# Performance work log

Hardware: AMD Instinct MI355X
Metric: run time of the kernel (lower is better)

Reference implementation:

```python
import jax, jax.numpy as jnp
import numpy as np

EMBED = 1024
B, I, J = 8, 2048, 2048
SCALE = EMBED ** -0.5


def setup_inputs() -> dict:
    key = jax.random.key(0)
    ks = jax.random.split(key, 5)
    s = EMBED ** -0.5  # init scale for weights
    return {
        "q_in": jax.random.normal(ks[0], (B, I, EMBED), dtype=jnp.float32),
        "k_v": jax.random.normal(ks[1], (B, J, EMBED), dtype=jnp.float32),
        "Wq": jax.random.normal(ks[2], (EMBED, EMBED), dtype=jnp.float32) * s,
        "bq": jnp.zeros((EMBED,), dtype=jnp.float32),
        "Wk": jax.random.normal(ks[3], (EMBED, EMBED), dtype=jnp.float32) * s,
        "bk": jnp.zeros((EMBED,), dtype=jnp.float32),
        "Wv": jax.random.normal(ks[4], (EMBED, EMBED), dtype=jnp.float32) * s,
        "bv": jnp.zeros((EMBED,), dtype=jnp.float32),
    }


def reference(q_in, k_v, Wq, bq, Wk, bk, Wv, bv):
    # Linear projections (torch Linear: x @ W.T + b; here W stored as [in, out])
    q = q_in @ Wq + bq            # [b, i, d]
    k = k_v @ Wk + bk             # [b, j, d]
    v = k_v @ Wv + bv             # [b, j, d]
    sim = jnp.einsum('bid,bjd->bij', q, k) * SCALE  # [b, i, j]
    attn = jax.nn.softmax(sim, axis=-1)
    # dropout with drop_rate=0.0 is identity
    out = jnp.einsum('bij,bjd->bid', attn, v)       # [b, i, d]
    return out
```

## Files before the change

### kernel.cpp

```cpp
#include <hip/hip_runtime.h>
#include <hip/hip_bf16.h>


#define BATCH 8
#define SEQ   2048
#define EMB   1024
#define SC2   0.045084222f

typedef __attribute__((ext_vector_type(8))) short bf16x8;
typedef __attribute__((ext_vector_type(4))) float f32x4;
typedef __attribute__((ext_vector_type(4))) unsigned short u16x4;
typedef __attribute__((ext_vector_type(8))) unsigned short u16x8;
typedef __attribute__((ext_vector_type(4))) float fl4;

__device__ __forceinline__ unsigned short f2bf(float f) {
    unsigned u = __builtin_bit_cast(unsigned, f);
    unsigned r = u + 0x7fffu + ((u >> 16) & 1u);
    return (unsigned short)(r >> 16);
}
__device__ __forceinline__ float bf2f(unsigned short s) {
    return __builtin_bit_cast(float, ((unsigned)s) << 16);
}
__device__ __forceinline__ void gload16(const unsigned short* g, unsigned short* l) {
    __builtin_amdgcn_global_load_lds(
        (const __attribute__((address_space(1))) void*)g,
        (__attribute__((address_space(3))) void*)l, 16, 0, 0);
}

__global__ __launch_bounds__(256)
void convert_all(const float* __restrict__ q_in, const float* __restrict__ k_v,
                 const float* __restrict__ Wq, const float* __restrict__ Wk,
                 const float* __restrict__ Wv,
                 unsigned short* __restrict__ qbin, unsigned short* __restrict__ kvbin,
                 unsigned short* __restrict__ Wt)
{
    const int bid = blockIdx.x;
    const int tid = threadIdx.x;
    if (bid < 4096) {
        const size_t N = (size_t)BATCH * SEQ * EMB;
        size_t idx = ((size_t)bid * 256 + tid) * 8;
        const size_t stride = (size_t)4096 * 256 * 8;
        for (; idx < N; idx += stride) {
            fl4 a0 = *(const fl4*)&q_in[idx];
            fl4 a1 = *(const fl4*)&q_in[idx + 4];
            fl4 b0 = *(const fl4*)&k_v[idx];
            fl4 b1 = *(const fl4*)&k_v[idx + 4];
            u16x8 ua, ub;
#pragma unroll
            for (int i = 0; i < 4; i++) {
                ua[i] = f2bf(a0[i]); ua[i + 4] = f2bf(a1[i]);
                ub[i] = f2bf(b0[i]); ub[i + 4] = f2bf(b1[i]);
            }
            *(u16x8*)&qbin[idx] = ua;
            *(u16x8*)&kvbin[idx] = ub;
        }
    } else {
        const int b2 = bid - 4096;
        const int wsel = b2 >> 8, rest = b2 & 255;
        const float* W = (wsel == 0) ? Wq : (wsel == 1) ? Wk : Wv;
        unsigned short* O = Wt + (size_t)wsel * EMB * EMB;
        const int k0 = (rest >> 4) * 64;
        const int n0 = (rest & 15) * 64;
        __shared__ unsigned short l[64 * 65];
#pragma unroll
        for (int it = 0; it < 16; it++) {
            const int lin = it * 256 + tid;
            const int k = lin >> 6, n = lin & 63;
            l[n * 65 + k] = f2bf(W[(size_t)(k0 + k) * EMB + n0 + n]);
        }
        __syncthreads();
#pragma unroll
        for (int it = 0; it < 16; it++) {
            const int lin = it * 256 + tid;
            const int n = lin >> 6, k = lin & 63;
            O[(size_t)(n0 + n) * EMB + k0 + k] = l[n * 65 + k];
        }
    }
}

__device__ __forceinline__ void stageT(const unsigned short* lanebase, size_t rstride,
                                       unsigned short* lwave) {
#pragma unroll
    for (int i = 0; i < 2; i++)
        gload16(lanebase + (size_t)(i * 128) * rstride, lwave + i * 4096);
}

#define PIPE_TILE(SLOT, DO_STAGE, STAGE_A_BASE, STAGE_A_LDS, STAGE_B_BASE, STAGE_B_LDS) \
    {                                                                           \
        const unsigned short* pa = &sA[SLOT][0];                                \
        const unsigned short* pb = &sB[SLOT][0];                                \
        bf16x8 a0 = *(bf16x8*)&pa[aoff0];                                       \
        bf16x8 a1 = *(bf16x8*)&pa[aoff0 + 512];                                 \
        bf16x8 a2 = *(bf16x8*)&pa[aoff0 + 1024];                                \
        bf16x8 a3 = *(bf16x8*)&pa[aoff0 + 1536];                                \
        bf16x8 a4 = *(bf16x8*)&pa[aoff0 + 2048];                                \
        bf16x8 a5 = *(bf16x8*)&pa[aoff0 + 2560];                                \
        bf16x8 a6 = *(bf16x8*)&pa[aoff0 + 3072];                                \
        bf16x8 a7 = *(bf16x8*)&pa[aoff0 + 3584];                                \
        bf16x8 bv0 = *(bf16x8*)&pb[boff0];                                      \
        bf16x8 bv1 = *(bf16x8*)&pb[boff0 + 512];                                \
        bf16x8 bv2 = *(bf16x8*)&pb[boff0 + 1024];                               \
        bf16x8 bv3 = *(bf16x8*)&pb[boff0 + 1536];                               \
        if (DO_STAGE) stageT(STAGE_A_BASE, strideA, STAGE_A_LDS);               \
        __builtin_amdgcn_s_setprio(1);                                          \
        acc[0][0] = __builtin_amdgcn_mfma_f32_16x16x32_bf16(a0, bv0, acc[0][0], 0, 0, 0); \
        acc[0][1] = __builtin_amdgcn_mfma_f32_16x16x32_bf16(a0, bv1, acc[0][1], 0, 0, 0); \
        acc[0][2] = __builtin_amdgcn_mfma_f32_16x16x32_bf16(a0, bv2, acc[0][2], 0, 0, 0); \
        acc[0][3] = __builtin_amdgcn_mfma_f32_16x16x32_bf16(a0, bv3, acc[0][3], 0, 0, 0); \
        acc[1][0] = __builtin_amdgcn_mfma_f32_16x16x32_bf16(a1, bv0, acc[1][0], 0, 0, 0); \
        acc[1][1] = __builtin_amdgcn_mfma_f32_16x16x32_bf16(a1, bv1, acc[1][1], 0, 0, 0); \
        acc[1][2] = __builtin_amdgcn_mfma_f32_16x16x32_bf16(a1, bv2, acc[1][2], 0, 0, 0); \
        acc[1][3] = __builtin_amdgcn_mfma_f32_16x16x32_bf16(a1, bv3, acc[1][3], 0, 0, 0); \
        acc[2][0] = __builtin_amdgcn_mfma_f32_16x16x32_bf16(a2, bv0, acc[2][0], 0, 0, 0); \
        acc[2][1] = __builtin_amdgcn_mfma_f32_16x16x32_bf16(a2, bv1, acc[2][1], 0, 0, 0); \
        acc[2][2] = __builtin_amdgcn_mfma_f32_16x16x32_bf16(a2, bv2, acc[2][2], 0, 0, 0); \
        acc[2][3] = __builtin_amdgcn_mfma_f32_16x16x32_bf16(a2, bv3, acc[2][3], 0, 0, 0); \
        acc[3][0] = __builtin_amdgcn_mfma_f32_16x16x32_bf16(a3, bv0, acc[3][0], 0, 0, 0); \
        acc[3][1] = __builtin_amdgcn_mfma_f32_16x16x32_bf16(a3, bv1, acc[3][1], 0, 0, 0); \
        acc[3][2] = __builtin_amdgcn_mfma_f32_16x16x32_bf16(a3, bv2, acc[3][2], 0, 0, 0); \
        acc[3][3] = __builtin_amdgcn_mfma_f32_16x16x32_bf16(a3, bv3, acc[3][3], 0, 0, 0); \
        __builtin_amdgcn_s_setprio(0);                                          \
        if (DO_STAGE) stageT(STAGE_B_BASE, strideB, STAGE_B_LDS);               \
        __builtin_amdgcn_s_setprio(1);                                          \
        acc[4][0] = __builtin_amdgcn_mfma_f32_16x16x32_bf16(a4, bv0, acc[4][0], 0, 0, 0); \
        acc[4][1] = __builtin_amdgcn_mfma_f32_16x16x32_bf16(a4, bv1, acc[4][1], 0, 0, 0); \
        acc[4][2] = __builtin_amdgcn_mfma_f32_16x16x32_bf16(a4, bv2, acc[4][2], 0, 0, 0); \
        acc[4][3] = __builtin_amdgcn_mfma_f32_16x16x32_bf16(a4, bv3, acc[4][3], 0, 0, 0); \
        acc[5][0] = __builtin_amdgcn_mfma_f32_16x16x32_bf16(a5, bv0, acc[5][0], 0, 0, 0); \
        acc[5][1] = __builtin_amdgcn_mfma_f32_16x16x32_bf16(a5, bv1, acc[5][1], 0, 0, 0); \
        acc[5][2] = __builtin_amdgcn_mfma_f32_16x16x32_bf16(a5, bv2, acc[5][2], 0, 0, 0); \
        acc[5][3] = __builtin_amdgcn_mfma_f32_16x16x32_bf16(a5, bv3, acc[5][3], 0, 0, 0); \
        acc[6][0] = __builtin_amdgcn_mfma_f32_16x16x32_bf16(a6, bv0, acc[6][0], 0, 0, 0); \
        acc[6][1] = __builtin_amdgcn_mfma_f32_16x16x32_bf16(a6, bv1, acc[6][1], 0, 0, 0); \
        acc[6][2] = __builtin_amdgcn_mfma_f32_16x16x32_bf16(a6, bv2, acc[6][2], 0, 0, 0); \
        acc[6][3] = __builtin_amdgcn_mfma_f32_16x16x32_bf16(a6, bv3, acc[6][3], 0, 0, 0); \
        acc[7][0] = __builtin_amdgcn_mfma_f32_16x16x32_bf16(a7, bv0, acc[7][0], 0, 0, 0); \
        acc[7][1] = __builtin_amdgcn_mfma_f32_16x16x32_bf16(a7, bv1, acc[7][1], 0, 0, 0); \
        acc[7][2] = __builtin_amdgcn_mfma_f32_16x16x32_bf16(a7, bv2, acc[7][2], 0, 0, 0); \
        acc[7][3] = __builtin_amdgcn_mfma_f32_16x16x32_bf16(a7, bv3, acc[7][3], 0, 0, 0); \
        __builtin_amdgcn_s_setprio(0);                                          \
        asm volatile("s_waitcnt vmcnt(4)" ::: "memory");                        \
        __builtin_amdgcn_s_barrier();                                           \
        __builtin_amdgcn_sched_barrier(0);                                      \
    }

__device__ __forceinline__ void pipe_gemm(
    const unsigned short* __restrict__ Asrc,
    const unsigned short* __restrict__ Bsrc,
    const size_t strideA, const size_t strideB, const int NT,
    unsigned short (*sA)[8192], unsigned short (*sB)[8192],
    const int lwave, const int aoff0, const int boff0,
    f32x4 acc[8][4])
{
    stageT(Asrc, strideA, &sA[0][lwave]);
    stageT(Bsrc, strideB, &sB[0][lwave]);
    stageT(Asrc + 32, strideA, &sA[1][lwave]);
    stageT(Bsrc + 32, strideB, &sB[1][lwave]);
    asm volatile("s_waitcnt vmcnt(4)" ::: "memory");
    __builtin_amdgcn_s_barrier();
    __builtin_amdgcn_sched_barrier(0);

    for (int T = 0; T < NT; ++T) {
        const int s = T & 3;
        const int doStage = (T + 2 < NT);
        const int s2 = (T + 2) & 3;
        PIPE_TILE(s, doStage, Asrc + (T + 2) * 32, &sA[s2][lwave],
                  Bsrc + (T + 2) * 32, &sB[s2][lwave]);
    }
}

#define PIPE_PREAMBLE                                                     \
    __shared__ unsigned short sMem[65536];                    \
    unsigned short (*sA)[8192] = (unsigned short (*)[8192])sMem;          \
    unsigned short (*sB)[8192] = (unsigned short (*)[8192])(sMem + 32768);\
    const int tid = threadIdx.x, lane = tid & 63;                         \
    const int wid = tid >> 6, wr = wid >> 2, wn = wid & 3;                \
    const int r = lane & 15, g = lane >> 4;                               \
    const int lwave = (wid << 9);                                         \
    const int scol = ((tid & 3) ^ ((tid >> 3) & 3)) * 8;                  \
    const int gsw = (g ^ ((r >> 1) & 3)) * 8;                             \
    const int aoff0 = (wr * 128 + r) * 32 + gsw;                          \
    const int boff0 = (wn * 64 + r) * 32 + gsw;                           \
    f32x4 acc[8][4];                                                      \
    _Pragma("unroll") for (int i_ = 0; i_ < 8; i_++)                      \
    _Pragma("unroll") for (int j_ = 0; j_ < 4; j_++) acc[i_][j_] = (f32x4)0.0f;

__device__ __forceinline__ void lds_flush_bf16(const unsigned short* sP,
                                               unsigned short* gbase,
                                               size_t gstride, int tid)
{
    const int lane = tid & 63, wv = tid >> 6;
    const int rowsel = lane >> 5, jj = lane & 31;
#pragma unroll
    for (int it = 0; it < 16; ++it) {
        const int row = it * 16 + wv * 2 + rowsel;
        const int byte = row * 512 + ((jj * 16) ^ ((row & 7) << 4));
        u16x8 v = *(const u16x8*)((const char*)sP + byte);
        *(u16x8*)&gbase[(size_t)row * gstride + jj * 8] = v;
    }
}

__global__ __launch_bounds__(512, 1)
void proj_all(const unsigned short* __restrict__ Wt,
              const unsigned short* __restrict__ qbin,
              const unsigned short* __restrict__ kvbin,
              const float* __restrict__ bq, const float* __restrict__ bk,
              const float* __restrict__ bv,
              unsigned short* __restrict__ qb, unsigned short* __restrict__ kb,
              unsigned short* __restrict__ vt)
{
    PIPE_PREAMBLE
    const int bid = blockIdx.x;
    const size_t strideA = EMB, strideB = EMB;
    const unsigned short* Asrc;
    const unsigned short* Bsrc;
    int d0 = 0, i0 = 0, m0 = 0, n0 = 0;
    const bool qrole = (bid < 256);
    if (qrole) {
        const int lid = (bid & 7) * 32 + (bid >> 3);
        d0 = (lid & 3) * 256; i0 = (lid >> 2) * 256;
        Asrc = Wt + (size_t)(d0 + (tid >> 2)) * EMB + scol;
        Bsrc = qbin + (size_t)(i0 + (tid >> 2)) * EMB + scol;
    } else {
        const int b2 = bid - 256;
        const int lid = (b2 & 7) * 64 + (b2 >> 3);
        n0 = (lid & 7) * 256; m0 = (lid >> 3) * 256;
        Asrc = kvbin + (size_t)(m0 + (tid >> 2)) * EMB + scol;
        Bsrc = Wt + (size_t)EMB * EMB + (size_t)(n0 + (tid >> 2)) * EMB + scol;
    }

    pipe_gemm(Asrc, Bsrc, strideA, strideB, EMB / 32, sA, sB, lwave, aoff0, boff0, acc);

    if (qrole) {
#pragma unroll
        for (int mm = 0; mm < 8; mm++) {
            const int colb = wr * 128 + mm * 16 + g * 4;
            const fl4 b4 = *(const fl4*)&bq[d0 + colb];
#pragma unroll
            for (int n = 0; n < 4; n++) {
                const int row = wn * 64 + n * 16 + r;
                u16x4 u;
#pragma unroll
                for (int c = 0; c < 4; c++) u[c] = f2bf(acc[mm][n][c] + b4[c]);
                const int byte = row * 512 + ((colb * 2) ^ ((row & 7) << 4));
                *(u16x4*)((char*)sMem + byte) = u;
            }
        }
        __syncthreads();
        lds_flush_bf16(sMem, qb + (size_t)i0 * EMB + d0, EMB, tid);
    } else {
        const int b = m0 >> 11;
        const int j0l = m0 & 2047;
        if (n0 < 1024) {
#pragma unroll
            for (int mm = 0; mm < 8; mm++) {
                const int ibase = m0 + wr * 128 + mm * 16 + g * 4;
#pragma unroll
                for (int n = 0; n < 4; n++) {
                    const int col = n0 + wn * 64 + n * 16 + r;
                    const float bb = bk[col];
#pragma unroll
                    for (int c = 0; c < 4; c++)
                        kb[(size_t)(ibase + c) * EMB + col] = f2bf(acc[mm][n][c] + bb);
                }
            }
        } else {
#pragma unroll
            for (int mm = 0; mm < 8; mm++) {
                const int colb = wr * 128 + mm * 16 + g * 4;
#pragma unroll
                for (int n = 0; n < 4; n++) {
                    const int row = wn * 64 + n * 16 + r;
                    const float bb = bv[n0 - 1024 + row];
                    u16x4 u;
#pragma unroll
                    for (int c = 0; c < 4; c++) u[c] = f2bf(acc[mm][n][c] + bb);
                    const int byte = row * 512 + ((colb * 2) ^ ((row & 7) << 4));
                    *(u16x4*)((char*)sMem + byte) = u;
                }
            }
            __syncthreads();
            lds_flush_bf16(sMem, vt + ((size_t)b * EMB + (n0 - 1024)) * SEQ + j0l,
                           SEQ, tid);
        }
    }
}

__global__ __launch_bounds__(512, 1)
void qk256_kernel(const unsigned short* __restrict__ qb,
                  const unsigned short* __restrict__ kb,
                  unsigned short* __restrict__ P,
                  float* __restrict__ Ppart)
{
    PIPE_PREAMBLE
    const int bid = blockIdx.x;
    const int lid = (bid & 7) * 64 + (bid >> 3);
    const int b = lid >> 6, jt = (lid >> 3) & 7, it = lid & 7;
    const int j0 = jt * 256, i0 = it * 256;
    const size_t strideA = EMB, strideB = EMB;
    const unsigned short* Ag = kb + (size_t)b * SEQ * EMB;
    const unsigned short* Bg = qb + (size_t)b * SEQ * EMB;
    const unsigned short* Asrc = Ag + (size_t)(j0 + (tid >> 2)) * EMB + scol;
    const unsigned short* Bsrc = Bg + (size_t)(i0 + (tid >> 2)) * EMB + scol;

    pipe_gemm(Asrc, Bsrc, strideA, strideB, EMB / 32, sA, sB, lwave, aoff0, boff0, acc);

    float ps[4] = {0.f, 0.f, 0.f, 0.f};
#pragma unroll
    for (int mm = 0; mm < 8; mm++) {
        const int colb = wr * 128 + mm * 16 + g * 4;
#pragma unroll
        for (int n = 0; n < 4; n++) {
            const int row = wn * 64 + n * 16 + r;
            u16x4 u;
#pragma unroll
            for (int c = 0; c < 4; c++) {
                const float p = exp2f(acc[mm][n][c] * SC2);
                ps[n] += p;
                u[c] = f2bf(p);
            }
            const int byte = row * 512 + ((colb * 2) ^ ((row & 7) << 4));
            *(u16x4*)((char*)sMem + byte) = u;
        }
    }
#pragma unroll
    for (int n = 0; n < 4; n++) {
        ps[n] += __shfl_xor(ps[n], 16);
        ps[n] += __shfl_xor(ps[n], 32);
    }
    if (g == 0) {
        const int slot = jt * 2 + wr;
        float* pp = Ppart + (size_t)slot * (BATCH * SEQ) + (size_t)b * SEQ;
#pragma unroll
        for (int n = 0; n < 4; n++)
            pp[i0 + wn * 64 + n * 16 + r] = ps[n];
    }
    __syncthreads();
    unsigned short* Pb = P + (size_t)b * SEQ * SEQ;
    lds_flush_bf16(sMem, Pb + (size_t)i0 * SEQ + j0, SEQ, tid);
}

__global__ __launch_bounds__(512, 1)
void pv256_kernel(const unsigned short* __restrict__ P,
                  const unsigned short* __restrict__ vt,
                  const float* __restrict__ Ppart,
                  float* __restrict__ out)
{
    PIPE_PREAMBLE
    const int bid = blockIdx.x;
    const int lid = (bid & 7) * 32 + (bid >> 3);
    const int b = lid >> 5, it = (lid >> 2) & 7, dt = lid & 3;
    const int d0 = dt * 256, i0 = it * 256;
    const size_t strideA = SEQ, strideB = SEQ;
    const unsigned short* Ag = vt + (size_t)b * EMB * SEQ;
    const unsigned short* Bg = P + (size_t)b * SEQ * SEQ;
    const unsigned short* Asrc = Ag + (size_t)(d0 + (tid >> 2)) * SEQ + scol;
    const unsigned short* Bsrc = Bg + (size_t)(i0 + (tid >> 2)) * SEQ + scol;

    float inv[4];
#pragma unroll
    for (int n = 0; n < 4; n++) {
        const int row = b * SEQ + i0 + wn * 64 + n * 16 + r;
        float s = 0.f;
#pragma unroll
        for (int slot = 0; slot < 16; slot++)
            s += Ppart[(size_t)slot * (BATCH * SEQ) + row];
        inv[n] = 1.0f / s;
    }

    pipe_gemm(Asrc, Bsrc, strideA, strideB, SEQ / 32, sA, sB, lwave, aoff0, boff0, acc);

    float* ob = out + (size_t)b * SEQ * EMB;
    float* sF = (float*)sMem;
#pragma unroll
    for (int h = 0; h < 2; h++) {
        if (wr == h) {
#pragma unroll
            for (int mm = 0; mm < 8; mm++) {
                const int colb = mm * 16 + g * 4;
#pragma unroll
                for (int n = 0; n < 4; n++) {
                    const int row = wn * 64 + n * 16 + r;
                    fl4 o;
#pragma unroll
                    for (int c = 0; c < 4; c++) o[c] = acc[mm][n][c] * inv[n];
                    const int byte = row * 512 + ((colb * 4) ^ ((row & 7) << 4));
                    *(fl4*)((char*)sF + byte) = o;
                }
            }
        }
        __syncthreads();
        {
            const int rowsel = lane >> 5, jj = lane & 31;
#pragma unroll
            for (int itx = 0; itx < 16; ++itx) {
                const int row = itx * 16 + wid * 2 + rowsel;
                const int byte = row * 512 + ((jj * 16) ^ ((row & 7) << 4));
                fl4 v = *(const fl4*)((const char*)sF + byte);
                *(fl4*)&ob[(size_t)(i0 + row) * EMB + d0 + h * 128 + jj * 4] = v;
            }
        }
        if (h == 0) __syncthreads();
    }
}

extern "C" void kernel_launch(void* const* d_in, const int* in_sizes, int n_in,
                              void* d_out, int out_size, void* d_ws, size_t ws_size,
                              hipStream_t stream)
{
    const float* q_in = (const float*)d_in[0];
    const float* k_v  = (const float*)d_in[1];
    const float* Wq   = (const float*)d_in[2];
    const float* bq   = (const float*)d_in[3];
    const float* Wk   = (const float*)d_in[4];
    const float* bk   = (const float*)d_in[5];
    const float* Wv   = (const float*)d_in[6];
    const float* bv   = (const float*)d_in[7];
    float* out = (float*)d_out;

    char* ws = (char*)d_ws;
    unsigned short* qbin = (unsigned short*)(ws);
    unsigned short* kvbin= (unsigned short*)(ws + (size_t)33554432);
    unsigned short* P    = (unsigned short*)(ws);
    unsigned short* qb   = (unsigned short*)(ws + (size_t)67108864);
    unsigned short* kb   = (unsigned short*)(ws + (size_t)100663296);
    unsigned short* vt   = (unsigned short*)(ws + (size_t)134217728);
    unsigned short* Wt   = (unsigned short*)(ws + (size_t)167772160);
    float*          Ppart= (float*)(ws + (size_t)174063616);

    convert_all<<<4864, 256, 0, stream>>>(q_in, k_v, Wq, Wk, Wv, qbin, kvbin, Wt);
    proj_all<<<768, 512, 0, stream>>>(Wt, qbin, kvbin, bq, bk, bv, qb, kb, vt);
    qk256_kernel<<<512, 512, 0, stream>>>(qb, kb, P, Ppart);
    pv256_kernel<<<256, 512, 0, stream>>>(P, vt, Ppart, out);
}
```

Before: 293.9 us.

## Deepen GEMM pipeline with register-prefetched LDS fragments and three-tile global prefetch

Restructures the pipelined GEMM loop. The next tile's A and B fragments are read from LDS into registers during the current tile's MFMAs, ping-ponging between two register sets with the loop unrolled by two. Global-to-LDS staging now runs three tiles ahead instead of two, with both A and B issued together before the MFMA block. The aim is to hide LDS read latency and global load latency behind matrix math, at the cost of about 64 extra VGPRs and an assumption that the tile count is even.

```diff
diff --git a/kernel.cpp b/kernel.cpp
--- a/kernel.cpp
+++ b/kernel.cpp
@@ -85,59 +85,64 @@
         gload16(lanebase + (size_t)(i * 128) * rstride, lwave + i * 4096);
 }
 
-#define PIPE_TILE(SLOT, DO_STAGE, STAGE_A_BASE, STAGE_A_LDS, STAGE_B_BASE, STAGE_B_LDS) \
+#define PIPE_TILE(T, CA0,CA1,CA2,CA3,CB0,CB1,CB2,CB3,                           \
+                     NA0,NA1,NA2,NA3,NB0,NB1,NB2,NB3)                           \
     {                                                                           \
-        const unsigned short* pa = &sA[SLOT][0];                                \
-        const unsigned short* pb = &sB[SLOT][0];                                \
-        bf16x8 a0 = *(bf16x8*)&pa[aoff0];                                       \
-        bf16x8 a1 = *(bf16x8*)&pa[aoff0 + 512];                                 \
-        bf16x8 a2 = *(bf16x8*)&pa[aoff0 + 1024];                                \
-        bf16x8 a3 = *(bf16x8*)&pa[aoff0 + 1536];                                \
-        bf16x8 a4 = *(bf16x8*)&pa[aoff0 + 2048];                                \
-        bf16x8 a5 = *(bf16x8*)&pa[aoff0 + 2560];                                \
-        bf16x8 a6 = *(bf16x8*)&pa[aoff0 + 3072];                                \
-        bf16x8 a7 = *(bf16x8*)&pa[aoff0 + 3584];                                \
-        bf16x8 bv0 = *(bf16x8*)&pb[boff0];                                      \
-        bf16x8 bv1 = *(bf16x8*)&pb[boff0 + 512];                                \
-        bf16x8 bv2 = *(bf16x8*)&pb[boff0 + 1024];                               \
-        bf16x8 bv3 = *(bf16x8*)&pb[boff0 + 1536];                               \
-        if (DO_STAGE) stageT(STAGE_A_BASE, strideA, STAGE_A_LDS);               \
+        const int sc_ = (T) & 3, sn_ = ((T) + 1) & 3, ss_ = ((T) + 3) & 3;      \
+        const unsigned short* pc_ = &sA[sc_][0];                                \
+        bf16x8 x4 = *(bf16x8*)&pc_[aoff0 + 2048];                               \
+        bf16x8 x5 = *(bf16x8*)&pc_[aoff0 + 2560];                               \
+        bf16x8 x6 = *(bf16x8*)&pc_[aoff0 + 3072];                               \
+        bf16x8 x7 = *(bf16x8*)&pc_[aoff0 + 3584];                               \
+        if ((T) + 1 < NT) {                                                     \
+            const unsigned short* pa_ = &sA[sn_][0];                            \
+            const unsigned short* pb_ = &sB[sn_][0];                            \
+            NA0 = *(bf16x8*)&pa_[aoff0];                                        \
+            NA1 = *(bf16x8*)&pa_[aoff0 + 512];                                  \
+            NA2 = *(bf16x8*)&pa_[aoff0 + 1024];                                 \
+            NA3 = *(bf16x8*)&pa_[aoff0 + 1536];                                 \
+            NB0 = *(bf16x8*)&pb_[boff0];                                        \
+            NB1 = *(bf16x8*)&pb_[boff0 + 512];                                  \
+            NB2 = *(bf16x8*)&pb_[boff0 + 1024];                                 \
+            NB3 = *(bf16x8*)&pb_[boff0 + 1536];                                 \
+        }                                                                       \
+        if ((T) + 3 < NT) {                                                     \
+            stageT(Asrc + ((T) + 3) * 32, strideA, &sA[ss_][lwave]);            \
+            stageT(Bsrc + ((T) + 3) * 32, strideB, &sB[ss_][lwave]);            \
+        }                                                                       \
         __builtin_amdgcn_s_setprio(1);                                          \
-        acc[0][0] = __builtin_amdgcn_mfma_f32_16x16x32_bf16(a0, bv0, acc[0][0], 0, 0, 0); \
-        acc[0][1] = __builtin_amdgcn_mfma_f32_16x16x32_bf16(a0, bv1, acc[0][1], 0, 0, 0); \
-        acc[0][2] = __builtin_amdgcn_mfma_f32_16x16x32_bf16(a0, bv2, acc[0][2], 0, 0, 0); \
-        acc[0][3] = __builtin_amdgcn_mfma_f32_16x16x32_bf16(a0, bv3, acc[0][3], 0, 0, 0); \
-        acc[1][0] = __builtin_amdgcn_mfma_f32_16x16x32_bf16(a1, bv0, acc[1][0], 0, 0, 0); \
-        acc[1][1] = __builtin_amdgcn_mfma_f32_16x16x32_bf16(a1, bv1, acc[1][1], 0, 0, 0); \
-        acc[1][2] = __builtin_amdgcn_mfma_f32_16x16x32_bf16(a1, bv2, acc[1][2], 0, 0, 0); \
-        acc[1][3] = __builtin_amdgcn_mfma_f32_16x16x32_bf16(a1, bv3, acc[1][3], 0, 0, 0); \
-        acc[2][0] = __builtin_amdgcn_mfma_f32_16x16x32_bf16(a2, bv0, acc[2][0], 0, 0, 0); \
-        acc[2][1] = __builtin_amdgcn_mfma_f32_16x16x32_bf16(a2, bv1, acc[2][1], 0, 0, 0); \
-        acc[2][2] = __builtin_amdgcn_mfma_f32_16x16x32_bf16(a2, bv2, acc[2][2], 0, 0, 0); \
-        acc[2][3] = __builtin_amdgcn_mfma_f32_16x16x32_bf16(a2, bv3, acc[2][3], 0, 0, 0); \
-        acc[3][0] = __builtin_amdgcn_mfma_f32_16x16x32_bf16(a3, bv0, acc[3][0], 0, 0, 0); \
-        acc[3][1] = __builtin_amdgcn_mfma_f32_16x16x32_bf16(a3, bv1, acc[3][1], 0, 0, 0); \
-        acc[3][2] = __builtin_amdgcn_mfma_f32_16x16x32_bf16(a3, bv2, acc[3][2], 0, 0, 0); \
-        acc[3][3] = __builtin_amdgcn_mfma_f32_16x16x32_bf16(a3, bv3, acc[3][3], 0, 0, 0); \
-        __builtin_amdgcn_s_setprio(0);                                          \
-        if (DO_STAGE) stageT(STAGE_B_BASE, strideB, STAGE_B_LDS);               \
-        __builtin_amdgcn_s_setprio(1);                                          \
-        acc[4][0] = __builtin_amdgcn_mfma_f32_16x16x32_bf16(a4, bv0, acc[4][0], 0, 0, 0); \
-        acc[4][1] = __builtin_amdgcn_mfma_f32_16x16x32_bf16(a4, bv1, acc[4][1], 0, 0, 0); \
-        acc[4][2] = __builtin_amdgcn_mfma_f32_16x16x32_bf16(a4, bv2, acc[4][2], 0, 0, 0); \
-        acc[4][3] = __builtin_amdgcn_mfma_f32_16x16x32_bf16(a4, bv3, acc[4][3], 0, 0, 0); \
-        acc[5][0] = __builtin_amdgcn_mfma_f32_16x16x32_bf16(a5, bv0, acc[5][0], 0, 0, 0); \
-        acc[5][1] = __builtin_amdgcn_mfma_f32_16x16x32_bf16(a5, bv1, acc[5][1], 0, 0, 0); \
-        acc[5][2] = __builtin_amdgcn_mfma_f32_16x16x32_bf16(a5, bv2, acc[5][2], 0, 0, 0); \
-        acc[5][3] = __builtin_amdgcn_mfma_f32_16x16x32_bf16(a5, bv3, acc[5][3], 0, 0, 0); \
-        acc[6][0] = __builtin_amdgcn_mfma_f32_16x16x32_bf16(a6, bv0, acc[6][0], 0, 0, 0); \
-        acc[6][1] = __builtin_amdgcn_mfma_f32_16x16x32_bf16(a6, bv1, acc[6][1], 0, 0, 0); \
-        acc[6][2] = __builtin_amdgcn_mfma_f32_16x16x32_bf16(a6, bv2, acc[6][2], 0, 0, 0); \
-        acc[6][3] = __builtin_amdgcn_mfma_f32_16x16x32_bf16(a6, bv3, acc[6][3], 0, 0, 0); \
-        acc[7][0] = __builtin_amdgcn_mfma_f32_16x16x32_bf16(a7, bv0, acc[7][0], 0, 0, 0); \
-        acc[7][1] = __builtin_amdgcn_mfma_f32_16x16x32_bf16(a7, bv1, acc[7][1], 0, 0, 0); \
-        acc[7][2] = __builtin_amdgcn_mfma_f32_16x16x32_bf16(a7, bv2, acc[7][2], 0, 0, 0); \
-        acc[7][3] = __builtin_amdgcn_mfma_f32_16x16x32_bf16(a7, bv3, acc[7][3], 0, 0, 0); \
+        acc[0][0] = __builtin_amdgcn_mfma_f32_16x16x32_bf16(CA0, CB0, acc[0][0], 0, 0, 0); \
+        acc[0][1] = __builtin_amdgcn_mfma_f32_16x16x32_bf16(CA0, CB1, acc[0][1], 0, 0, 0); \
+        acc[0][2] = __builtin_amdgcn_mfma_f32_16x16x32_bf16(CA0, CB2, acc[0][2], 0, 0, 0); \
+        acc[0][3] = __builtin_amdgcn_mfma_f32_16x16x32_bf16(CA0, CB3, acc[0][3], 0, 0, 0); \
+        acc[1][0] = __builtin_amdgcn_mfma_f32_16x16x32_bf16(CA1, CB0, acc[1][0], 0, 0, 0); \
+        acc[1][1] = __builtin_amdgcn_mfma_f32_16x16x32_bf16(CA1, CB1, acc[1][1], 0, 0, 0); \
+        acc[1][2] = __builtin_amdgcn_mfma_f32_16x16x32_bf16(CA1, CB2, acc[1][2], 0, 0, 0); \
+        acc[1][3] = __builtin_amdgcn_mfma_f32_16x16x32_bf16(CA1, CB3, acc[1][3], 0, 0, 0); \
+        acc[2][0] = __builtin_amdgcn_mfma_f32_16x16x32_bf16(CA2, CB0, acc[2][0], 0, 0, 0); \
+        acc[2][1] = __builtin_amdgcn_mfma_f32_16x16x32_bf16(CA2, CB1, acc[2][1], 0, 0, 0); \
+        acc[2][2] = __builtin_amdgcn_mfma_f32_16x16x32_bf16(CA2, CB2, acc[2][2], 0, 0, 0); \
+        acc[2][3] = __builtin_amdgcn_mfma_f32_16x16x32_bf16(CA2, CB3, acc[2][3], 0, 0, 0); \
+        acc[3][0] = __builtin_amdgcn_mfma_f32_16x16x32_bf16(CA3, CB0, acc[3][0], 0, 0, 0); \
+        acc[3][1] = __builtin_amdgcn_mfma_f32_16x16x32_bf16(CA3, CB1, acc[3][1], 0, 0, 0); \
+        acc[3][2] = __builtin_amdgcn_mfma_f32_16x16x32_bf16(CA3, CB2, acc[3][2], 0, 0, 0); \
+        acc[3][3] = __builtin_amdgcn_mfma_f32_16x16x32_bf16(CA3, CB3, acc[3][3], 0, 0, 0); \
+        acc[4][0] = __builtin_amdgcn_mfma_f32_16x16x32_bf16(x4, CB0, acc[4][0], 0, 0, 0); \
+        acc[4][1] = __builtin_amdgcn_mfma_f32_16x16x32_bf16(x4, CB1, acc[4][1], 0, 0, 0); \
+        acc[4][2] = __builtin_amdgcn_mfma_f32_16x16x32_bf16(x4, CB2, acc[4][2], 0, 0, 0); \
+        acc[4][3] = __builtin_amdgcn_mfma_f32_16x16x32_bf16(x4, CB3, acc[4][3], 0, 0, 0); \
+        acc[5][0] = __builtin_amdgcn_mfma_f32_16x16x32_bf16(x5, CB0, acc[5][0], 0, 0, 0); \
+        acc[5][1] = __builtin_amdgcn_mfma_f32_16x16x32_bf16(x5, CB1, acc[5][1], 0, 0, 0); \
+        acc[5][2] = __builtin_amdgcn_mfma_f32_16x16x32_bf16(x5, CB2, acc[5][2], 0, 0, 0); \
+        acc[5][3] = __builtin_amdgcn_mfma_f32_16x16x32_bf16(x5, CB3, acc[5][3], 0, 0, 0); \
+        acc[6][0] = __builtin_amdgcn_mfma_f32_16x16x32_bf16(x6, CB0, acc[6][0], 0, 0, 0); \
+        acc[6][1] = __builtin_amdgcn_mfma_f32_16x16x32_bf16(x6, CB1, acc[6][1], 0, 0, 0); \
+        acc[6][2] = __builtin_amdgcn_mfma_f32_16x16x32_bf16(x6, CB2, acc[6][2], 0, 0, 0); \
+        acc[6][3] = __builtin_amdgcn_mfma_f32_16x16x32_bf16(x6, CB3, acc[6][3], 0, 0, 0); \
+        acc[7][0] = __builtin_amdgcn_mfma_f32_16x16x32_bf16(x7, CB0, acc[7][0], 0, 0, 0); \
+        acc[7][1] = __builtin_amdgcn_mfma_f32_16x16x32_bf16(x7, CB1, acc[7][1], 0, 0, 0); \
+        acc[7][2] = __builtin_amdgcn_mfma_f32_16x16x32_bf16(x7, CB2, acc[7][2], 0, 0, 0); \
+        acc[7][3] = __builtin_amdgcn_mfma_f32_16x16x32_bf16(x7, CB3, acc[7][3], 0, 0, 0); \
         __builtin_amdgcn_s_setprio(0);                                          \
         asm volatile("s_waitcnt vmcnt(4)" ::: "memory");                        \
         __builtin_amdgcn_s_barrier();                                           \
@@ -152,20 +157,31 @@
     const int lwave, const int aoff0, const int boff0,
     f32x4 acc[8][4])
 {
-    stageT(Asrc, strideA, &sA[0][lwave]);
-    stageT(Bsrc, strideB, &sB[0][lwave]);
+    stageT(Asrc,      strideA, &sA[0][lwave]);
+    stageT(Bsrc,      strideB, &sB[0][lwave]);
     stageT(Asrc + 32, strideA, &sA[1][lwave]);
     stageT(Bsrc + 32, strideB, &sB[1][lwave]);
+    stageT(Asrc + 64, strideA, &sA[2][lwave]);
+    stageT(Bsrc + 64, strideB, &sB[2][lwave]);
     asm volatile("s_waitcnt vmcnt(4)" ::: "memory");
     __builtin_amdgcn_s_barrier();
     __builtin_amdgcn_sched_barrier(0);
 
-    for (int T = 0; T < NT; ++T) {
-        const int s = T & 3;
-        const int doStage = (T + 2 < NT);
-        const int s2 = (T + 2) & 3;
-        PIPE_TILE(s, doStage, Asrc + (T + 2) * 32, &sA[s2][lwave],
-                  Bsrc + (T + 2) * 32, &sB[s2][lwave]);
+    bf16x8 Pa0, Pa1, Pa2, Pa3, Pb0, Pb1, Pb2, Pb3;
+    bf16x8 Qa0, Qa1, Qa2, Qa3, Qb0, Qb1, Qb2, Qb3;
+    {
+        const unsigned short* pa = &sA[0][0];
+        const unsigned short* pb = &sB[0][0];
+        Pa0 = *(bf16x8*)&pa[aoff0];        Pa1 = *(bf16x8*)&pa[aoff0 + 512];
+        Pa2 = *(bf16x8*)&pa[aoff0 + 1024]; Pa3 = *(bf16x8*)&pa[aoff0 + 1536];
+        Pb0 = *(bf16x8*)&pb[boff0];        Pb1 = *(bf16x8*)&pb[boff0 + 512];
+        Pb2 = *(bf16x8*)&pb[boff0 + 1024]; Pb3 = *(bf16x8*)&pb[boff0 + 1536];
+    }
+    for (int T = 0; T < NT; T += 2) {
+        PIPE_TILE(T,     Pa0,Pa1,Pa2,Pa3,Pb0,Pb1,Pb2,Pb3,
+                         Qa0,Qa1,Qa2,Qa3,Qb0,Qb1,Qb2,Qb3);
+        PIPE_TILE(T + 1, Qa0,Qa1,Qa2,Qa3,Qb0,Qb1,Qb2,Qb3,
+                         Pa0,Pa1,Pa2,Pa3,Pb0,Pb1,Pb2,Pb3);
     }
 }
 
```

Result: slower. 308.9 us (+5.1%).

## Fuse fp32-to-bf16 activation conversion into projection GEMM loader

Applied to the files above, without the earlier changes.

Drops the separate pass that converted q_in and k_v to bf16. The projection GEMM now loads fp32 activations into registers, packs them with v_cvt_pk_bf16_f32, and writes them to LDS inside a new mixed pipeline. Weights are still staged through the async global-to-LDS path. This removes a full read and write of the activation tensors, at the cost of a more complex register-staged pipeline with twice the global read bytes per tile. The last pipeline tile now waits for vmcnt(0), so the drain is also fixed.

```diff
diff --git a/kernel.cpp b/kernel.cpp
--- a/kernel.cpp
+++ b/kernel.cpp
@@ -11,6 +11,7 @@
 typedef __attribute__((ext_vector_type(4))) float f32x4;
 typedef __attribute__((ext_vector_type(4))) unsigned short u16x4;
 typedef __attribute__((ext_vector_type(8))) unsigned short u16x8;
+typedef __attribute__((ext_vector_type(4))) unsigned int u32x4;
 typedef __attribute__((ext_vector_type(4))) float fl4;
 
 __device__ __forceinline__ unsigned short f2bf(float f) {
@@ -21,6 +22,11 @@
 __device__ __forceinline__ float bf2f(unsigned short s) {
     return __builtin_bit_cast(float, ((unsigned)s) << 16);
 }
+__device__ __forceinline__ unsigned cvtpk(float a, float b) {
+    unsigned r;
+    asm("v_cvt_pk_bf16_f32 %0, %1, %2" : "=v"(r) : "v"(a), "v"(b));
+    return r;
+}
 __device__ __forceinline__ void gload16(const unsigned short* g, unsigned short* l) {
     __builtin_amdgcn_global_load_lds(
         (const __attribute__((address_space(1))) void*)g,
@@ -28,53 +34,28 @@
 }
 
 __global__ __launch_bounds__(256)
-void convert_all(const float* __restrict__ q_in, const float* __restrict__ k_v,
-                 const float* __restrict__ Wq, const float* __restrict__ Wk,
-                 const float* __restrict__ Wv,
-                 unsigned short* __restrict__ qbin, unsigned short* __restrict__ kvbin,
-                 unsigned short* __restrict__ Wt)
-{
-    const int bid = blockIdx.x;
+void convert_w(const float* __restrict__ Wq, const float* __restrict__ Wk,
+               const float* __restrict__ Wv, unsigned short* __restrict__ Wt)
+{
+    const int wsel = blockIdx.y;
+    const float* W = (wsel == 0) ? Wq : (wsel == 1) ? Wk : Wv;
+    unsigned short* O = Wt + (size_t)wsel * EMB * EMB;
+    const int k0 = (blockIdx.x >> 4) * 64;
+    const int n0 = (blockIdx.x & 15) * 64;
+    __shared__ unsigned short l[64 * 65];
     const int tid = threadIdx.x;
-    if (bid < 4096) {
-        const size_t N = (size_t)BATCH * SEQ * EMB;
-        size_t idx = ((size_t)bid * 256 + tid) * 8;
-        const size_t stride = (size_t)4096 * 256 * 8;
-        for (; idx < N; idx += stride) {
-            fl4 a0 = *(const fl4*)&q_in[idx];
-            fl4 a1 = *(const fl4*)&q_in[idx + 4];
-            fl4 b0 = *(const fl4*)&k_v[idx];
-            fl4 b1 = *(const fl4*)&k_v[idx + 4];
-            u16x8 ua, ub;
-#pragma unroll
-            for (int i = 0; i < 4; i++) {
-                ua[i] = f2bf(a0[i]); ua[i + 4] = f2bf(a1[i]);
-                ub[i] = f2bf(b0[i]); ub[i + 4] = f2bf(b1[i]);
-            }
-            *(u16x8*)&qbin[idx] = ua;
-            *(u16x8*)&kvbin[idx] = ub;
-        }
-    } else {
-        const int b2 = bid - 4096;
-        const int wsel = b2 >> 8, rest = b2 & 255;
-        const float* W = (wsel == 0) ? Wq : (wsel == 1) ? Wk : Wv;
-        unsigned short* O = Wt + (size_t)wsel * EMB * EMB;
-        const int k0 = (rest >> 4) * 64;
-        const int n0 = (rest & 15) * 64;
-        __shared__ unsigned short l[64 * 65];
-#pragma unroll
-        for (int it = 0; it < 16; it++) {
-            const int lin = it * 256 + tid;
-            const int k = lin >> 6, n = lin & 63;
-            l[n * 65 + k] = f2bf(W[(size_t)(k0 + k) * EMB + n0 + n]);
-        }
-        __syncthreads();
-#pragma unroll
-        for (int it = 0; it < 16; it++) {
-            const int lin = it * 256 + tid;
-            const int n = lin >> 6, k = lin & 63;
-            O[(size_t)(n0 + n) * EMB + k0 + k] = l[n * 65 + k];
-        }
+#pragma unroll
+    for (int it = 0; it < 16; it++) {
+        const int lin = it * 256 + tid;
+        const int k = lin >> 6, n = lin & 63;
+        l[n * 65 + k] = f2bf(W[(size_t)(k0 + k) * EMB + n0 + n]);
+    }
+    __syncthreads();
+#pragma unroll
+    for (int it = 0; it < 16; it++) {
+        const int lin = it * 256 + tid;
+        const int n = lin >> 6, k = lin & 63;
+        O[(size_t)(n0 + n) * EMB + k0 + k] = l[n * 65 + k];
     }
 }
 
@@ -85,8 +66,43 @@
         gload16(lanebase + (size_t)(i * 128) * rstride, lwave + i * 4096);
 }
 
-#define PIPE_TILE(SLOT, DO_STAGE, STAGE_A_BASE, STAGE_A_LDS, STAGE_B_BASE, STAGE_B_LDS) \
-    {                                                                           \
+#define MFMA16_LO(A0,A1,A2,A3)                                                  \
+        acc[0][0] = __builtin_amdgcn_mfma_f32_16x16x32_bf16(A0, bv0, acc[0][0], 0, 0, 0); \
+        acc[0][1] = __builtin_amdgcn_mfma_f32_16x16x32_bf16(A0, bv1, acc[0][1], 0, 0, 0); \
+        acc[0][2] = __builtin_amdgcn_mfma_f32_16x16x32_bf16(A0, bv2, acc[0][2], 0, 0, 0); \
+        acc[0][3] = __builtin_amdgcn_mfma_f32_16x16x32_bf16(A0, bv3, acc[0][3], 0, 0, 0); \
+        acc[1][0] = __builtin_amdgcn_mfma_f32_16x16x32_bf16(A1, bv0, acc[1][0], 0, 0, 0); \
+        acc[1][1] = __builtin_amdgcn_mfma_f32_16x16x32_bf16(A1, bv1, acc[1][1], 0, 0, 0); \
+        acc[1][2] = __builtin_amdgcn_mfma_f32_16x16x32_bf16(A1, bv2, acc[1][2], 0, 0, 0); \
+        acc[1][3] = __builtin_amdgcn_mfma_f32_16x16x32_bf16(A1, bv3, acc[1][3], 0, 0, 0); \
+        acc[2][0] = __builtin_amdgcn_mfma_f32_16x16x32_bf16(A2, bv0, acc[2][0], 0, 0, 0); \
+        acc[2][1] = __builtin_amdgcn_mfma_f32_16x16x32_bf16(A2, bv1, acc[2][1], 0, 0, 0); \
+        acc[2][2] = __builtin_amdgcn_mfma_f32_16x16x32_bf16(A2, bv2, acc[2][2], 0, 0, 0); \
+        acc[2][3] = __builtin_amdgcn_mfma_f32_16x16x32_bf16(A2, bv3, acc[2][3], 0, 0, 0); \
+        acc[3][0] = __builtin_amdgcn_mfma_f32_16x16x32_bf16(A3, bv0, acc[3][0], 0, 0, 0); \
+        acc[3][1] = __builtin_amdgcn_mfma_f32_16x16x32_bf16(A3, bv1, acc[3][1], 0, 0, 0); \
+        acc[3][2] = __builtin_amdgcn_mfma_f32_16x16x32_bf16(A3, bv2, acc[3][2], 0, 0, 0); \
+        acc[3][3] = __builtin_amdgcn_mfma_f32_16x16x32_bf16(A3, bv3, acc[3][3], 0, 0, 0);
+
+#define MFMA16_HI(A4,A5,A6,A7)                                                  \
+        acc[4][0] = __builtin_amdgcn_mfma_f32_16x16x32_bf16(A4, bv0, acc[4][0], 0, 0, 0); \
+        acc[4][1] = __builtin_amdgcn_mfma_f32_16x16x32_bf16(A4, bv1, acc[4][1], 0, 0, 0); \
+        acc[4][2] = __builtin_amdgcn_mfma_f32_16x16x32_bf16(A4, bv2, acc[4][2], 0, 0, 0); \
+        acc[4][3] = __builtin_amdgcn_mfma_f32_16x16x32_bf16(A4, bv3, acc[4][3], 0, 0, 0); \
+        acc[5][0] = __builtin_amdgcn_mfma_f32_16x16x32_bf16(A5, bv0, acc[5][0], 0, 0, 0); \
+        acc[5][1] = __builtin_amdgcn_mfma_f32_16x16x32_bf16(A5, bv1, acc[5][1], 0, 0, 0); \
+        acc[5][2] = __builtin_amdgcn_mfma_f32_16x16x32_bf16(A5, bv2, acc[5][2], 0, 0, 0); \
+        acc[5][3] = __builtin_amdgcn_mfma_f32_16x16x32_bf16(A5, bv3, acc[5][3], 0, 0, 0); \
+        acc[6][0] = __builtin_amdgcn_mfma_f32_16x16x32_bf16(A6, bv0, acc[6][0], 0, 0, 0); \
+        acc[6][1] = __builtin_amdgcn_mfma_f32_16x16x32_bf16(A6, bv1, acc[6][1], 0, 0, 0); \
+        acc[6][2] = __builtin_amdgcn_mfma_f32_16x16x32_bf16(A6, bv2, acc[6][2], 0, 0, 0); \
+        acc[6][3] = __builtin_amdgcn_mfma_f32_16x16x32_bf16(A6, bv3, acc[6][3], 0, 0, 0); \
+        acc[7][0] = __builtin_amdgcn_mfma_f32_16x16x32_bf16(A7, bv0, acc[7][0], 0, 0, 0); \
+        acc[7][1] = __builtin_amdgcn_mfma_f32_16x16x32_bf16(A7, bv1, acc[7][1], 0, 0, 0); \
+        acc[7][2] = __builtin_amdgcn_mfma_f32_16x16x32_bf16(A7, bv2, acc[7][2], 0, 0, 0); \
+        acc[7][3] = __builtin_amdgcn_mfma_f32_16x16x32_bf16(A7, bv3, acc[7][3], 0, 0, 0);
+
+#define FRAG_READS(SLOT)                                                        \
         const unsigned short* pa = &sA[SLOT][0];                                \
         const unsigned short* pb = &sB[SLOT][0];                                \
         bf16x8 a0 = *(bf16x8*)&pa[aoff0];                                       \
@@ -100,49 +116,7 @@
         bf16x8 bv0 = *(bf16x8*)&pb[boff0];                                      \
         bf16x8 bv1 = *(bf16x8*)&pb[boff0 + 512];                                \
         bf16x8 bv2 = *(bf16x8*)&pb[boff0 + 1024];                               \
-        bf16x8 bv3 = *(bf16x8*)&pb[boff0 + 1536];                               \
-        if (DO_STAGE) stageT(STAGE_A_BASE, strideA, STAGE_A_LDS);               \
-        __builtin_amdgcn_s_setprio(1);                                          \
-        acc[0][0] = __builtin_amdgcn_mfma_f32_16x16x32_bf16(a0, bv0, acc[0][0], 0, 0, 0); \
-        acc[0][1] = __builtin_amdgcn_mfma_f32_16x16x32_bf16(a0, bv1, acc[0][1], 0, 0, 0); \
-        acc[0][2] = __builtin_amdgcn_mfma_f32_16x16x32_bf16(a0, bv2, acc[0][2], 0, 0, 0); \
-        acc[0][3] = __builtin_amdgcn_mfma_f32_16x16x32_bf16(a0, bv3, acc[0][3], 0, 0, 0); \
-        acc[1][0] = __builtin_amdgcn_mfma_f32_16x16x32_bf16(a1, bv0, acc[1][0], 0, 0, 0); \
-        acc[1][1] = __builtin_amdgcn_mfma_f32_16x16x32_bf16(a1, bv1, acc[1][1], 0, 0, 0); \
-        acc[1][2] = __builtin_amdgcn_mfma_f32_16x16x32_bf16(a1, bv2, acc[1][2], 0, 0, 0); \
-        acc[1][3] = __builtin_amdgcn_mfma_f32_16x16x32_bf16(a1, bv3, acc[1][3], 0, 0, 0); \
-        acc[2][0] = __builtin_amdgcn_mfma_f32_16x16x32_bf16(a2, bv0, acc[2][0], 0, 0, 0); \
-        acc[2][1] = __builtin_amdgcn_mfma_f32_16x16x32_bf16(a2, bv1, acc[2][1], 0, 0, 0); \
-        acc[2][2] = __builtin_amdgcn_mfma_f32_16x16x32_bf16(a2, bv2, acc[2][2], 0, 0, 0); \
-        acc[2][3] = __builtin_amdgcn_mfma_f32_16x16x32_bf16(a2, bv3, acc[2][3], 0, 0, 0); \
-        acc[3][0] = __builtin_amdgcn_mfma_f32_16x16x32_bf16(a3, bv0, acc[3][0], 0, 0, 0); \
-        acc[3][1] = __builtin_amdgcn_mfma_f32_16x16x32_bf16(a3, bv1, acc[3][1], 0, 0, 0); \
-        acc[3][2] = __builtin_amdgcn_mfma_f32_16x16x32_bf16(a3, bv2, acc[3][2], 0, 0, 0); \
-        acc[3][3] = __builtin_amdgcn_mfma_f32_16x16x32_bf16(a3, bv3, acc[3][3], 0, 0, 0); \
-        __builtin_amdgcn_s_setprio(0);                                          \
-        if (DO_STAGE) stageT(STAGE_B_BASE, strideB, STAGE_B_LDS);               \
-        __builtin_amdgcn_s_setprio(1);                                          \
-        acc[4][0] = __builtin_amdgcn_mfma_f32_16x16x32_bf16(a4, bv0, acc[4][0], 0, 0, 0); \
-        acc[4][1] = __builtin_amdgcn_mfma_f32_16x16x32_bf16(a4, bv1, acc[4][1], 0, 0, 0); \
-        acc[4][2] = __builtin_amdgcn_mfma_f32_16x16x32_bf16(a4, bv2, acc[4][2], 0, 0, 0); \
-        acc[4][3] = __builtin_amdgcn_mfma_f32_16x16x32_bf16(a4, bv3, acc[4][3], 0, 0, 0); \
-        acc[5][0] = __builtin_amdgcn_mfma_f32_16x16x32_bf16(a5, bv0, acc[5][0], 0, 0, 0); \
-        acc[5][1] = __builtin_amdgcn_mfma_f32_16x16x32_bf16(a5, bv1, acc[5][1], 0, 0, 0); \
-        acc[5][2] = __builtin_amdgcn_mfma_f32_16x16x32_bf16(a5, bv2, acc[5][2], 0, 0, 0); \
-        acc[5][3] = __builtin_amdgcn_mfma_f32_16x16x32_bf16(a5, bv3, acc[5][3], 0, 0, 0); \
-        acc[6][0] = __builtin_amdgcn_mfma_f32_16x16x32_bf16(a6, bv0, acc[6][0], 0, 0, 0); \
-        acc[6][1] = __builtin_amdgcn_mfma_f32_16x16x32_bf16(a6, bv1, acc[6][1], 0, 0, 0); \
-        acc[6][2] = __builtin_amdgcn_mfma_f32_16x16x32_bf16(a6, bv2, acc[6][2], 0, 0, 0); \
-        acc[6][3] = __builtin_amdgcn_mfma_f32_16x16x32_bf16(a6, bv3, acc[6][3], 0, 0, 0); \
-        acc[7][0] = __builtin_amdgcn_mfma_f32_16x16x32_bf16(a7, bv0, acc[7][0], 0, 0, 0); \
-        acc[7][1] = __builtin_amdgcn_mfma_f32_16x16x32_bf16(a7, bv1, acc[7][1], 0, 0, 0); \
-        acc[7][2] = __builtin_amdgcn_mfma_f32_16x16x32_bf16(a7, bv2, acc[7][2], 0, 0, 0); \
-        acc[7][3] = __builtin_amdgcn_mfma_f32_16x16x32_bf16(a7, bv3, acc[7][3], 0, 0, 0); \
-        __builtin_amdgcn_s_setprio(0);                                          \
-        asm volatile("s_waitcnt vmcnt(4)" ::: "memory");                        \
-        __builtin_amdgcn_s_barrier();                                           \
-        __builtin_amdgcn_sched_barrier(0);                                      \
-    }
+        bf16x8 bv3 = *(bf16x8*)&pb[boff0 + 1536];
 
 __device__ __forceinline__ void pipe_gemm(
     const unsigned short* __restrict__ Asrc,
@@ -164,8 +138,92 @@
         const int s = T & 3;
         const int doStage = (T + 2 < NT);
         const int s2 = (T + 2) & 3;
-        PIPE_TILE(s, doStage, Asrc + (T + 2) * 32, &sA[s2][lwave],
-                  Bsrc + (T + 2) * 32, &sB[s2][lwave]);
+        {
+            FRAG_READS(s)
+            if (doStage) stageT(Asrc + (T + 2) * 32, strideA, &sA[s2][lwave]);
+            __builtin_amdgcn_s_setprio(1);
+            MFMA16_LO(a0, a1, a2, a3)
+            __builtin_amdgcn_s_setprio(0);
+            if (doStage) stageT(Bsrc + (T + 2) * 32, strideB, &sB[s2][lwave]);
+            __builtin_amdgcn_s_setprio(1);
+            MFMA16_HI(a4, a5, a6, a7)
+            __builtin_amdgcn_s_setprio(0);
+            if (doStage) { asm volatile("s_waitcnt vmcnt(4)" ::: "memory"); }
+            else         { asm volatile("s_waitcnt vmcnt(0)" ::: "memory"); }
+            __builtin_amdgcn_s_barrier();
+            __builtin_amdgcn_sched_barrier(0);
+        }
+    }
+}
+
+#define ISSUEF(TT, R0, R1, R2, R3)                                              \
+    {                                                                           \
+        const float* fb_ = Fsrc + (size_t)(TT) * 32;                            \
+        R0 = *(const fl4*)fb_;                                                  \
+        R1 = *(const fl4*)(fb_ + 4);                                            \
+        R2 = *(const fl4*)(fb_ + 128 * strideF);                                \
+        R3 = *(const fl4*)(fb_ + 128 * strideF + 4);                            \
+    }
+#define WRITEF(SLOT, R0, R1, R2, R3)                                            \
+    {                                                                           \
+        unsigned short* d_ = &sF[SLOT][0] + tid * 8;                            \
+        u32x4 w0, w1;                                                           \
+        w0[0] = cvtpk(R0[0], R0[1]); w0[1] = cvtpk(R0[2], R0[3]);               \
+        w0[2] = cvtpk(R1[0], R1[1]); w0[3] = cvtpk(R1[2], R1[3]);               \
+        w1[0] = cvtpk(R2[0], R2[1]); w1[1] = cvtpk(R2[2], R2[3]);               \
+        w1[2] = cvtpk(R3[0], R3[1]); w1[3] = cvtpk(R3[2], R3[3]);               \
+        *(u32x4*)d_ = w0;                                                       \
+        *(u32x4*)(d_ + 4096) = w1;                                              \
+    }
+
+template <bool F32A>
+__device__ __forceinline__ void pipe_gemm_mx(
+    const float* __restrict__ Fsrc,
+    const unsigned short* __restrict__ Gsrc,
+    const size_t strideF, const size_t strideG, const int NT,
+    unsigned short (*sA)[8192], unsigned short (*sB)[8192],
+    const int lwave, const int aoff0, const int boff0, const int tid,
+    f32x4 acc[8][4])
+{
+    unsigned short (*sF)[8192] = F32A ? sA : sB;
+    unsigned short (*sG)[8192] = F32A ? sB : sA;
+
+    fl4 t0, t1, t2, t3, rf0, rf1, rf2, rf3;
+    ISSUEF(0, t0, t1, t2, t3);
+    ISSUEF(1, rf0, rf1, rf2, rf3);
+    __builtin_amdgcn_sched_barrier(0);
+    stageT(Gsrc,      strideG, &sG[0][lwave]);
+    stageT(Gsrc + 32, strideG, &sG[1][lwave]);
+    asm volatile("s_waitcnt vmcnt(2)" ::: "memory");
+    WRITEF(0, t0, t1, t2, t3);
+    asm volatile("s_waitcnt lgkmcnt(0)" ::: "memory");
+    __builtin_amdgcn_s_barrier();
+    __builtin_amdgcn_sched_barrier(0);
+
+    for (int T = 0; T < NT; ++T) {
+        const int s = T & 3;
+        const int sw = (T + 1) & 3;
+        const int s2 = (T + 2) & 3;
+        const int wrPre = (T + 1 < NT);
+        const int doLd  = (T + 2 < NT);
+        {
+            asm volatile("s_waitcnt vmcnt(2)" ::: "memory");
+            if (wrPre) { WRITEF(sw, rf0, rf1, rf2, rf3); }
+            if (doLd)  { ISSUEF(T + 2, rf0, rf1, rf2, rf3); }
+            __builtin_amdgcn_sched_barrier(0);
+            if (doLd)  stageT(Gsrc + (T + 2) * 32, strideG, &sG[s2][lwave]);
+            FRAG_READS(s)
+            __builtin_amdgcn_s_setprio(1);
+            MFMA16_LO(a0, a1, a2, a3)
+            __builtin_amdgcn_s_setprio(0);
+            __builtin_amdgcn_s_setprio(1);
+            MFMA16_HI(a4, a5, a6, a7)
+            __builtin_amdgcn_s_setprio(0);
+            if (doLd) { asm volatile("s_waitcnt vmcnt(6) lgkmcnt(0)" ::: "memory"); }
+            else      { asm volatile("s_waitcnt vmcnt(0) lgkmcnt(0)" ::: "memory"); }
+            __builtin_amdgcn_s_barrier();
+            __builtin_amdgcn_sched_barrier(0);
+        }
     }
 }
 
@@ -202,8 +260,8 @@
 
 __global__ __launch_bounds__(512, 1)
 void proj_all(const unsigned short* __restrict__ Wt,
-              const unsigned short* __restrict__ qbin,
-              const unsigned short* __restrict__ kvbin,
+              const float* __restrict__ q_in,
+              const float* __restrict__ k_v,
               const float* __restrict__ bq, const float* __restrict__ bk,
               const float* __restrict__ bv,
               unsigned short* __restrict__ qb, unsigned short* __restrict__ kb,
@@ -211,25 +269,25 @@
 {
     PIPE_PREAMBLE
     const int bid = blockIdx.x;
-    const size_t strideA = EMB, strideB = EMB;
-    const unsigned short* Asrc;
-    const unsigned short* Bsrc;
     int d0 = 0, i0 = 0, m0 = 0, n0 = 0;
     const bool qrole = (bid < 256);
     if (qrole) {
         const int lid = (bid & 7) * 32 + (bid >> 3);
         d0 = (lid & 3) * 256; i0 = (lid >> 2) * 256;
-        Asrc = Wt + (size_t)(d0 + (tid >> 2)) * EMB + scol;
-        Bsrc = qbin + (size_t)(i0 + (tid >> 2)) * EMB + scol;
+        const unsigned short* Gsrc = Wt + (size_t)(d0 + (tid >> 2)) * EMB + scol;
+        const float* Fsrc = q_in + (size_t)(i0 + (tid >> 2)) * EMB + scol;
+        pipe_gemm_mx<false>(Fsrc, Gsrc, EMB, EMB, EMB / 32,
+                            sA, sB, lwave, aoff0, boff0, tid, acc);
     } else {
         const int b2 = bid - 256;
         const int lid = (b2 & 7) * 64 + (b2 >> 3);
         n0 = (lid & 7) * 256; m0 = (lid >> 3) * 256;
-        Asrc = kvbin + (size_t)(m0 + (tid >> 2)) * EMB + scol;
-        Bsrc = Wt + (size_t)EMB * EMB + (size_t)(n0 + (tid >> 2)) * EMB + scol;
-    }
-
-    pipe_gemm(Asrc, Bsrc, strideA, strideB, EMB / 32, sA, sB, lwave, aoff0, boff0, acc);
+        const float* Fsrc = k_v + (size_t)(m0 + (tid >> 2)) * EMB + scol;
+        const unsigned short* Gsrc = Wt + (size_t)EMB * EMB
+                                   + (size_t)(n0 + (tid >> 2)) * EMB + scol;
+        pipe_gemm_mx<true>(Fsrc, Gsrc, EMB, EMB, EMB / 32,
+                           sA, sB, lwave, aoff0, boff0, tid, acc);
+    }
 
     if (qrole) {
 #pragma unroll
@@ -297,13 +355,12 @@
     const int lid = (bid & 7) * 64 + (bid >> 3);
     const int b = lid >> 6, jt = (lid >> 3) & 7, it = lid & 7;
     const int j0 = jt * 256, i0 = it * 256;
-    const size_t strideA = EMB, strideB = EMB;
     const unsigned short* Ag = kb + (size_t)b * SEQ * EMB;
     const unsigned short* Bg = qb + (size_t)b * SEQ * EMB;
     const unsigned short* Asrc = Ag + (size_t)(j0 + (tid >> 2)) * EMB + scol;
     const unsigned short* Bsrc = Bg + (size_t)(i0 + (tid >> 2)) * EMB + scol;
 
-    pipe_gemm(Asrc, Bsrc, strideA, strideB, EMB / 32, sA, sB, lwave, aoff0, boff0, acc);
+    pipe_gemm(Asrc, Bsrc, EMB, EMB, EMB / 32, sA, sB, lwave, aoff0, boff0, acc);
 
     float ps[4] = {0.f, 0.f, 0.f, 0.f};
 #pragma unroll
@@ -351,7 +408,6 @@
     const int lid = (bid & 7) * 32 + (bid >> 3);
     const int b = lid >> 5, it = (lid >> 2) & 7, dt = lid & 3;
     const int d0 = dt * 256, i0 = it * 256;
-    const size_t strideA = SEQ, strideB = SEQ;
     const unsigned short* Ag = vt + (size_t)b * EMB * SEQ;
     const unsigned short* Bg = P + (size_t)b * SEQ * SEQ;
     const unsigned short* Asrc = Ag + (size_t)(d0 + (tid >> 2)) * SEQ + scol;
@@ -368,7 +424,7 @@
         inv[n] = 1.0f / s;
     }
 
-    pipe_gemm(Asrc, Bsrc, strideA, strideB, SEQ / 32, sA, sB, lwave, aoff0, boff0, acc);
+    pipe_gemm(Asrc, Bsrc, SEQ, SEQ, SEQ / 32, sA, sB, lwave, aoff0, boff0, acc);
 
     float* ob = out + (size_t)b * SEQ * EMB;
     float* sF = (float*)sMem;
@@ -419,8 +475,6 @@
     float* out = (float*)d_out;
 
     char* ws = (char*)d_ws;
-    unsigned short* qbin = (unsigned short*)(ws);
-    unsigned short* kvbin= (unsigned short*)(ws + (size_t)33554432);
     unsigned short* P    = (unsigned short*)(ws);
     unsigned short* qb   = (unsigned short*)(ws + (size_t)67108864);
     unsigned short* kb   = (unsigned short*)(ws + (size_t)100663296);
@@ -428,8 +482,8 @@
     unsigned short* Wt   = (unsigned short*)(ws + (size_t)167772160);
     float*          Ppart= (float*)(ws + (size_t)174063616);
 
-    convert_all<<<4864, 256, 0, stream>>>(q_in, k_v, Wq, Wk, Wv, qbin, kvbin, Wt);
-    proj_all<<<768, 512, 0, stream>>>(Wt, qbin, kvbin, bq, bk, bv, qb, kb, vt);
+    convert_w<<<dim3(256, 3), 256, 0, stream>>>(Wq, Wk, Wv, Wt);
+    proj_all<<<768, 512, 0, stream>>>(Wt, q_in, k_v, bq, bk, bv, qb, kb, vt);
     qk256_kernel<<<512, 512, 0, stream>>>(qb, kb, P, Ppart);
     pv256_kernel<<<256, 512, 0, stream>>>(P, vt, Ppart, out);
 }
```

Measured after the change: 292.6 us. Within noise of the previous version (-0.5%).
